# Kernel optimization log

Measured on AMD Instinct MI355X. Metric: run time of the kernel, lower is better.

## Reference

```python
import jax, jax.numpy as jnp
import numpy as np

N = 100000
E = 1600000
D_IN, H1, H2 = 64, 128, 64
ATT = 32


def _mean_aggregate(feat, src, dst, num_nodes):
    # gather source features per edge, scatter-sum to destinations, divide by in-degree
    summed = jax.ops.segment_sum(feat[src], dst, num_segments=num_nodes)  # [N, d]
    deg = jax.ops.segment_sum(jnp.ones((src.shape[0],), feat.dtype), dst, num_segments=num_nodes)
    return summed / jnp.maximum(deg, 1.0)[:, None]


def setup_inputs() -> dict:
    key = jax.random.key(0)
    ks = jax.random.split(key, 16)
    x = jax.random.normal(ks[0], (N, D_IN), dtype=jnp.float32)
    edge_index = jax.random.randint(ks[1], (2, E), 0, N, dtype=jnp.int64)

    def lin(k, fan_in, fan_out):
        bound = 1.0 / np.sqrt(fan_in)
        return jax.random.uniform(k, (fan_in, fan_out), jnp.float32, -bound, bound)

    params = {
        'W1_l': lin(ks[2], D_IN, H1), 'W1_r': lin(ks[3], D_IN, H1),
        'b1': jnp.zeros((H1,), jnp.float32),
        'W2_l': lin(ks[4], H1, H2), 'W2_r': lin(ks[5], H1, H2),
        'b2': jnp.zeros((H2,), jnp.float32),
        'Wa': lin(ks[6], H2, ATT), 'ba': jnp.zeros((ATT,), jnp.float32),
        'ctx': jax.random.normal(ks[7], (ATT,), jnp.float32),
        'Wc1': lin(ks[8], H2, H2 // 2), 'bc1': jnp.zeros((H2 // 2,), jnp.float32),
        'Wc2': lin(ks[9], H2 // 2, 1), 'bc2': jnp.zeros((1,), jnp.float32),
    }
    return {'x': x, 'edge_index': edge_index, **params}


def reference(x, edge_index, W1_l, W1_r, b1, W2_l, W2_r, b2, Wa, ba, ctx, Wc1, bc1, Wc2, bc2):
    src, dst = edge_index[0], edge_index[1]
    ionm_alerts = x[:, -1]  # [N]

    # GraphSAGE layer 1 (mean aggr): lin_l(mean_neighbors) + lin_r(x_self)
    agg1 = _mean_aggregate(x, src, dst, N)
    h = jax.nn.relu(agg1 @ W1_l + b1 + x @ W1_r)  # [N, H1]
    # F.dropout(training=False) -> identity

    # GraphSAGE layer 2
    agg2 = _mean_aggregate(h, src, dst, N)
    h = jax.nn.relu(agg2 @ W2_l + b2 + h @ W2_r)  # [N, H2]

    # attention with IONM alert boost (+0.4)
    scores = jnp.tanh(h @ Wa + ba)            # [N, ATT]
    w = scores @ ctx + ionm_alerts * 0.4       # [N]
    w = jax.nn.softmax(w, axis=0)
    h = h * w[:, None]

    pooled = jnp.mean(h, axis=0, keepdims=True)  # [1, H2]

    # classifier head (Dropout identity in eval)
    z = jax.nn.relu(pooled @ Wc1 + bc1)
    return jax.nn.sigmoid(z @ Wc2 + bc2)  # [1, 1]
```

## Files before the change

### kernel.cpp

```cpp
#include <hip/hip_runtime.h>
#include <math.h>

#define N_NODES 100000
#define E_EDGES 1600000
#define D_IN 64
#define HID1 128
#define HID2 64
#define ATT 32
#define CAP 64
#define AT_STRIDE 136
#define NRANGE 4
#define RNODES (N_NODES / NRANGE)
#define NPART 64
#define XCAST_BLOCKS ((N_NODES * 16 + 255) / 256)
#define SCAT_BLOCKS 1024

typedef unsigned int uint32;
typedef unsigned short ushort;
typedef __attribute__((ext_vector_type(8))) short short8;
typedef __attribute__((ext_vector_type(4))) float float4v;

#define NTL(p) __builtin_nontemporal_load(&(p))

__device__ inline uint32 bf16rn(float f){ uint32 u = __float_as_uint(f); return (u + 0x7fffu + ((u >> 16) & 1u)) >> 16; }
__device__ inline uint32 packbf2(float a, float b){ return bf16rn(a) | (bf16rn(b) << 16); }

#if __has_builtin(__builtin_amdgcn_cvt_f32_fp8) && __has_builtin(__builtin_amdgcn_cvt_pk_fp8_f32)
#define HW_FP8 1
#endif

__device__ inline uint32 fp8_enc_sw(float f){
    float a = fabsf(f);
    uint32 s = (__float_as_uint(f) >> 24) & 0x80u;
    if (!(a >= 0.001953125f)) return s;
    if (a > 448.f) return s | 0x7Eu;
    if (a < 0.015625f){
        uint32 c = (uint32)rintf(a * 512.f);
        return s | c;
    }
    int e; float m = frexpf(a, &e);
    int E = e - 1;
    float mant = 2.f * m;
    uint32 mc = (uint32)rintf((mant - 1.f) * 8.f);
    uint32 Ec = (uint32)(E + 7);
    if (mc == 8u){ mc = 0u; Ec += 1u; }
    if (Ec >= 16u || (Ec == 15u && mc > 6u)) return s | 0x7Eu;
    return s | (Ec << 3) | mc;
}

__device__ inline float fp8_dec_sw(uint32 c){
    uint32 s = (c & 0x80u) << 24;
    uint32 E = (c >> 3) & 0xFu, m = c & 7u;
    float v;
    if (E == 0) v = (float)m * 0.001953125f;
    else v = __uint_as_float(((E + 120u) << 23) | (m << 20));
    return __uint_as_float(__float_as_uint(v) | s);
}

__device__ inline uint32 enc4(float a, float b, float c, float d){
#ifdef HW_FP8
    int r = __builtin_amdgcn_cvt_pk_fp8_f32(a, b, 0, false);
    r = __builtin_amdgcn_cvt_pk_fp8_f32(c, d, r, true);
    return (uint32)r;
#else
    return fp8_enc_sw(a) | (fp8_enc_sw(b) << 8) | (fp8_enc_sw(c) << 16) | (fp8_enc_sw(d) << 24);
#endif
}

__device__ inline void dec4acc(uint32 w, float& a0, float& a1, float& a2, float& a3){
#ifdef HW_FP8
    a0 += __builtin_amdgcn_cvt_f32_fp8((int)w, 0);
    a1 += __builtin_amdgcn_cvt_f32_fp8((int)w, 1);
    a2 += __builtin_amdgcn_cvt_f32_fp8((int)w, 2);
    a3 += __builtin_amdgcn_cvt_f32_fp8((int)w, 3);
#else
    a0 += fp8_dec_sw(w & 0xffu);
    a1 += fp8_dec_sw((w >> 8) & 0xffu);
    a2 += fp8_dec_sw((w >> 16) & 0xffu);
    a3 += fp8_dec_sw(w >> 24);
#endif
}

__global__ void k_mega(const float* __restrict__ x,
                       const int* __restrict__ src, const int* __restrict__ dst,
                       const float* __restrict__ W1l, const float* __restrict__ W1r,
                       const float* __restrict__ W2l, const float* __restrict__ W2r,
                       uint32* __restrict__ xb, uint32* __restrict__ xq,
                       uint32* __restrict__ vq,
                       ushort* __restrict__ wt1g, ushort* __restrict__ wt2g,
                       int* __restrict__ cnt, int* __restrict__ ssrc){
    int b = blockIdx.x, t = threadIdx.x;
    if (b < XCAST_BLOCKS){
        int i = b * 256 + t;
        if (i < N_NODES * 16){
            float4v v = NTL(((const float4v*)x)[i]);
            xb[2 * i]     = packbf2(v.x, v.y);
            xb[2 * i + 1] = packbf2(v.z, v.w);
            xq[i] = enc4(v.x, v.y, v.z, v.w);
        }
        return;
    }
    if (b < XCAST_BLOCKS + 2){
        int sub = b - XCAST_BLOCKS;
        ushort* dstp = (sub == 0) ? wt1g : wt2g;
        for (int idx = t; idx < 128 * 128; idx += 256){
            int nn = idx >> 7, kk = idx & 127;
            float v;
            if (sub == 0) v = (kk < 64) ? W1l[kk * 128 + nn] : W1r[(kk - 64) * 128 + nn];
            else          v = (nn < 64) ? W2l[kk * 64 + nn]  : W2r[kk * 64 + (nn - 64)];
            dstp[nn * 128 + kk] = (ushort)bf16rn(v);
        }
        if (sub == 0){
            if (t < 16) xq[(size_t)N_NODES * 16 + t] = 0u;
            else if (t < 32) vq[(size_t)N_NODES * 16 + (t - 16)] = 0u;
        }
        return;
    }
    int rel = b - (XCAST_BLOCKS + 2);
    int range = rel & (NRANGE - 1);
    int blk   = rel >> 2;
    int lo = range * RNODES, hi = lo + RNODES;
    int stride = (SCAT_BLOCKS >> 2) * 256;
    for (int i = blk * 256 + t; i < E_EDGES; i += stride){
        int d = NTL(dst[i]);
        if (d >= lo && d < hi){
            int pos = atomicAdd(&cnt[d], 1);
            if (pos < CAP) ssrc[d * CAP + pos] = NTL(src[i]);
        }
    }
}

__device__ inline void gather8_fp8(const uint32* __restrict__ tab,
                                   const int* __restrict__ ssrc,
                                   const int* __restrict__ cnt,
                                   int n0, int lane,
                                   float acc[8][4], int cct[8]){
    int q = lane >> 4, p = lane & 15;
    int nn = n0 + (lane & 7);
    int ccl_ = cnt[nn];
    int cc[8];
    #pragma unroll
    for (int j = 0; j < 8; j++){
        int c = __shfl(ccl_, j, 64);
        cct[j] = c;
        cc[j] = min(c, CAP);
    }
    #pragma unroll
    for (int j = 0; j < 8; j++){ acc[j][0] = acc[j][1] = acc[j][2] = acc[j][3] = 0.f; }
    int cmax = 0;
    #pragma unroll
    for (int j = 0; j < 8; j++) cmax = max(cmax, cc[j]);
    if (cmax == 0) return;
    int se[8];
    #pragma unroll
    for (int j = 0; j < 8; j++){
        se[j] = (lane < cc[j]) ? NTL(ssrc[(n0 + j) * CAP + lane]) : N_NODES;
    }
    int iters = (cmax + 3) >> 2;
    uint32 w[8];
    #pragma unroll
    for (int j = 0; j < 8; j++){
        int s = __shfl(se[j], q, 64);
        w[j] = tab[(uint32)s * 16u + p];
    }
    for (int it = 0; it < iters; it++){
        uint32 wn[8];
        bool more = (it + 1 < iters);
        int idxn = (it + 1) * 4 + q;
        if (more){
            #pragma unroll
            for (int j = 0; j < 8; j++){
                int s = __shfl(se[j], idxn, 64);
                wn[j] = tab[(uint32)s * 16u + p];
            }
        }
        #pragma unroll
        for (int j = 0; j < 8; j++)
            dec4acc(w[j], acc[j][0], acc[j][1], acc[j][2], acc[j][3]);
        if (more){
            #pragma unroll
            for (int j = 0; j < 8; j++) w[j] = wn[j];
        }
    }
    #pragma unroll
    for (int j = 0; j < 8; j++){
        acc[j][0] += __shfl_xor(acc[j][0], 16, 64); acc[j][1] += __shfl_xor(acc[j][1], 16, 64);
        acc[j][2] += __shfl_xor(acc[j][2], 16, 64); acc[j][3] += __shfl_xor(acc[j][3], 16, 64);
        acc[j][0] += __shfl_xor(acc[j][0], 32, 64); acc[j][1] += __shfl_xor(acc[j][1], 32, 64);
        acc[j][2] += __shfl_xor(acc[j][2], 32, 64); acc[j][3] += __shfl_xor(acc[j][3], 32, 64);
    }
}

__global__ __launch_bounds__(256) void k_layer1(
    const uint32* __restrict__ xq, const uint32* __restrict__ xb,
    const int* __restrict__ ssrc, const int* __restrict__ cnt,
    const ushort* __restrict__ wt1g, const ushort* __restrict__ wt2g,
    const float* __restrict__ b1, const float* __restrict__ b2,
    uint32* __restrict__ vq, float* __restrict__ r2f){
    __shared__ ushort smem[2 * 32 * AT_STRIDE];
    ushort* at  = smem;
    ushort* at2 = smem + 32 * AT_STRIDE;
    float* vstage = (float*)smem;
    int t = threadIdx.x, wave = t >> 6, lane = t & 63;
    int nb0 = blockIdx.x * 32;
    int n0 = nb0 + wave * 8;

    int m0 = t >> 3, ch = t & 7;
    uint4 xval = *(const uint4*)&xb[(size_t)(nb0 + m0) * 32 + ch * 4];

    float acc[8][4]; int cct[8];
    gather8_fp8(xq, ssrc, cnt, n0, lane, acc, cct);
    int p = lane & 15;
    if (lane < 16){
        #pragma unroll
        for (int j = 0; j < 8; j++){
            float inv = 1.f / fmaxf((float)cct[j], 1.f);
            uint2 o;
            o.x = packbf2(acc[j][0] * inv, acc[j][1] * inv);
            o.y = packbf2(acc[j][2] * inv, acc[j][3] * inv);
            *(uint2*)&at[(wave * 8 + j) * AT_STRIDE + 4 * p] = o;
        }
    }
    *(uint4*)((uint32*)(at + m0 * AT_STRIDE + 64) + ch * 4) = xval;
    __syncthreads();

    int cidx = lane & 15, quad = lane >> 4;
    int mt = wave >> 1;
    int nbase = (wave & 1) * 64;
    float4v c[4];
    #pragma unroll
    for (int nt = 0; nt < 4; nt++) c[nt] = (float4v){0.f,0.f,0.f,0.f};
    #pragma unroll
    for (int kt = 0; kt < 4; kt++){
        short8 a = *(short8*)(at + ((mt * 16 + cidx) * AT_STRIDE + kt * 32 + quad * 8));
        #pragma unroll
        for (int nt = 0; nt < 4; nt++){
            short8 b = *(const short8*)(wt1g + ((nbase + nt * 16 + cidx) * 128 + kt * 32 + quad * 8));
            c[nt] = __builtin_amdgcn_mfma_f32_16x16x32_bf16(a, b, c[nt], 0, 0, 0);
        }
    }
    #pragma unroll
    for (int nt = 0; nt < 4; nt++){
        float bb = b1[nbase + nt * 16 + cidx];
        #pragma unroll
        for (int i = 0; i < 4; i++){
            int row = quad * 4 + i;
            at2[(mt * 16 + row) * AT_STRIDE + nbase + nt * 16 + cidx] =
                (ushort)bf16rn(fmaxf(c[nt][i] + bb, 0.f));
        }
    }
    __syncthreads();
    #pragma unroll
    for (int nt = 0; nt < 4; nt++) c[nt] = (float4v){0.f,0.f,0.f,0.f};
    #pragma unroll
    for (int kt = 0; kt < 4; kt++){
        short8 a = *(short8*)(at2 + ((mt * 16 + cidx) * AT_STRIDE + kt * 32 + quad * 8));
        #pragma unroll
        for (int nt = 0; nt < 4; nt++){
            short8 b = *(const short8*)(wt2g + ((nbase + nt * 16 + cidx) * 128 + kt * 32 + quad * 8));
            c[nt] = __builtin_amdgcn_mfma_f32_16x16x32_bf16(a, b, c[nt], 0, 0, 0);
        }
    }
    if (nbase == 0){
        #pragma unroll
        for (int nt = 0; nt < 4; nt++){
            #pragma unroll
            for (int i = 0; i < 4; i++){
                int row = quad * 4 + i;
                vstage[(mt * 16 + row) * 65 + nt * 16 + cidx] = c[nt][i];
            }
        }
    } else {
        #pragma unroll
        for (int nt = 0; nt < 4; nt++){
            float bb = b2[nt * 16 + cidx];
            #pragma unroll
            for (int i = 0; i < 4; i++){
                int row = quad * 4 + i;
                size_t node = nb0 + mt * 16 + row;
                r2f[node * 64 + nt * 16 + cidx] = c[nt][i] + bb;
            }
        }
    }
    __syncthreads();
    {
        int m = t >> 3, u = t & 7;
        float f0 = vstage[m * 65 + 8 * u],     f1 = vstage[m * 65 + 8 * u + 1];
        float f2 = vstage[m * 65 + 8 * u + 2], f3 = vstage[m * 65 + 8 * u + 3];
        float f4 = vstage[m * 65 + 8 * u + 4], f5 = vstage[m * 65 + 8 * u + 5];
        float f6 = vstage[m * 65 + 8 * u + 6], f7 = vstage[m * 65 + 8 * u + 7];
        vq[(size_t)(nb0 + m) * 16 + 2 * u]     = enc4(f0, f1, f2, f3);
        vq[(size_t)(nb0 + m) * 16 + 2 * u + 1] = enc4(f4, f5, f6, f7);
    }
}

__global__ __launch_bounds__(256) void k_gather2f(
    const float* __restrict__ x, const uint32* __restrict__ vq,
    const int* __restrict__ ssrc, const int* __restrict__ cnt,
    const float* __restrict__ r2f,
    const float* __restrict__ Wa, const float* __restrict__ ba, const float* __restrict__ ctx,
    float* __restrict__ pooledP, float* __restrict__ Zpart){
    __shared__ float sh2[32][68];
    __shared__ float sew[32];
    __shared__ float sp[4][64];
    int t = threadIdx.x, wave = t >> 6, lane = t & 63;
    int bn0 = blockIdx.x * 32;
    int n0 = bn0 + wave * 8;
    float acc[8][4]; int cct[8];
    gather8_fp8(vq, ssrc, cnt, n0, lane, acc, cct);
    int p = lane & 15;
    if (lane < 16){
        #pragma unroll
        for (int j = 0; j < 8; j++){
            size_t nj = n0 + j;
            float inv = 1.f / fmaxf((float)cct[j], 1.f);
            float4v rr = NTL(*(const float4v*)&r2f[nj * 64 + 4 * p]);
            float4v hv;
            hv.x = fmaxf(acc[j][0] * inv + rr.x, 0.f);
            hv.y = fmaxf(acc[j][1] * inv + rr.y, 0.f);
            hv.z = fmaxf(acc[j][2] * inv + rr.z, 0.f);
            hv.w = fmaxf(acc[j][3] * inv + rr.w, 0.f);
            *(float4v*)&sh2[wave * 8 + j][4 * p] = hv;
        }
    }
    __syncthreads();
    int node = t >> 3;
    int c0 = (t & 7) * 4;
    float s0 = ba[c0], s1 = ba[c0 + 1], s2 = ba[c0 + 2], s3 = ba[c0 + 3];
    #pragma unroll 8
    for (int j = 0; j < 64; j++){
        float hv = sh2[node][j];
        s0 += hv * Wa[j * ATT + c0];
        s1 += hv * Wa[j * ATT + c0 + 1];
        s2 += hv * Wa[j * ATT + c0 + 2];
        s3 += hv * Wa[j * ATT + c0 + 3];
    }
    float pa = tanhf(s0) * ctx[c0] + tanhf(s1) * ctx[c0 + 1]
             + tanhf(s2) * ctx[c0 + 2] + tanhf(s3) * ctx[c0 + 3];
    #pragma unroll
    for (int off = 4; off >= 1; off >>= 1) pa += __shfl_down(pa, off, 8);
    if ((t & 7) == 0){
        int n = bn0 + node;
        float w = pa + NTL(x[(size_t)n * 64 + 63]) * 0.4f;
        sew[node] = expf(w);
    }
    __syncthreads();
    int j = t & 63, q = t >> 6;
    float p4 = 0.f;
    #pragma unroll
    for (int m = 0; m < 8; m++) p4 += sh2[q * 8 + m][j] * sew[q * 8 + m];
    sp[q][j] = p4;
    __syncthreads();
    if (t < 64){
        float s = sp[0][t] + sp[1][t] + sp[2][t] + sp[3][t];
        atomicAdd(&pooledP[(blockIdx.x & (NPART - 1)) * 64 + t], s);
    }
    if (t == 64){
        float z = 0.f;
        #pragma unroll
        for (int m = 0; m < 32; m++) z += sew[m];
        atomicAdd(&Zpart[blockIdx.x & (NPART - 1)], z);
    }
}

__global__ void k_final(const float* __restrict__ pooledP, const float* __restrict__ Zpart,
                        const float* __restrict__ Wc1, const float* __restrict__ bc1,
                        const float* __restrict__ Wc2, const float* __restrict__ bc2,
                        float* __restrict__ out){
    __shared__ float sp[64], sz[32];
    __shared__ float Zs;
    int t = threadIdx.x;
    float s = 0.f;
    for (int q = 0; q < NPART; q++) s += pooledP[q * 64 + t];
    if (t == 0){
        float z = 0.f;
        for (int q = 0; q < NPART; q++) z += Zpart[q];
        Zs = z;
    }
    __syncthreads();
    float scale = 1.0f / (Zs * (float)N_NODES);
    sp[t] = s * scale;
    __syncthreads();
    if (t < 32){
        float a = bc1[t];
        #pragma unroll 8
        for (int j = 0; j < 64; j++) a += sp[j] * Wc1[j * 32 + t];
        sz[t] = fmaxf(a, 0.f);
    }
    __syncthreads();
    if (t == 0){
        float a = bc2[0];
        #pragma unroll
        for (int i = 0; i < 32; i++) a += sz[i] * Wc2[i];
        out[0] = 1.0f / (1.0f + expf(-a));
    }
}

extern "C" void kernel_launch(void* const* d_in, const int* in_sizes, int n_in,
                              void* d_out, int out_size, void* d_ws, size_t ws_size,
                              hipStream_t stream) {
    const float* x   = (const float*)d_in[0];
    const int*   ei  = (const int*)d_in[1];
    const int*   src = ei;
    const int*   dst = ei + E_EDGES;
    const float* W1l = (const float*)d_in[2];
    const float* W1r = (const float*)d_in[3];
    const float* b1  = (const float*)d_in[4];
    const float* W2l = (const float*)d_in[5];
    const float* W2r = (const float*)d_in[6];
    const float* b2  = (const float*)d_in[7];
    const float* Wa  = (const float*)d_in[8];
    const float* ba  = (const float*)d_in[9];
    const float* ctx = (const float*)d_in[10];
    const float* Wc1 = (const float*)d_in[11];
    const float* bc1 = (const float*)d_in[12];
    const float* Wc2 = (const float*)d_in[13];
    const float* bc2 = (const float*)d_in[14];

    char* p = (char*)d_ws;
    int* cnt    = (int*)p;                 p += (size_t)N_NODES * 4;
    int* ssrc   = (int*)p;                 p += (size_t)N_NODES * CAP * 4;
    uint32* xb  = (uint32*)p;              p += (size_t)N_NODES * 32 * 4;
    uint32* xq  = (uint32*)p;              p += (size_t)(N_NODES + 1) * 16 * 4;
    uint32* vq  = (uint32*)p;              p += (size_t)(N_NODES + 1) * 16 * 4;
    float* r2f  = (float*)p;               p += (size_t)N_NODES * 64 * 4;
    ushort* wt1g = (ushort*)p;             p += 128 * 128 * 2;
    ushort* wt2g = (ushort*)p;             p += 128 * 128 * 2;
    float* pooledP = (float*)p;            p += NPART * 64 * 4;
    float* Zpart   = (float*)p;            p += NPART * 4;

    hipMemsetAsync(cnt, 0, (size_t)N_NODES * 4, stream);
    hipMemsetAsync(pooledP, 0, (NPART * 64 + NPART) * 4, stream);

    k_mega<<<XCAST_BLOCKS + 2 + SCAT_BLOCKS, 256, 0, stream>>>(
        x, src, dst, W1l, W1r, W2l, W2r, xb, xq, vq, wt1g, wt2g, cnt, ssrc);

    k_layer1<<<(N_NODES + 31) / 32, 256, 0, stream>>>(xq, xb, ssrc, cnt,
                                                      wt1g, wt2g, b1, b2, vq, r2f);
    k_gather2f<<<(N_NODES + 31) / 32, 256, 0, stream>>>(x, vq, ssrc, cnt, r2f,
                                                        Wa, ba, ctx, pooledP, Zpart);
    k_final<<<1, 64, 0, stream>>>(pooledP, Zpart, Wc1, bc1, Wc2, bc2, (float*)d_out);
}
```

Measured before the change: 341.9 us.

## Fuse final head into gather kernel via ticket, drop memset, prefetch indices deeper

The final classifier head moves into the last block of k_gather2f, which is picked with an atomic ticket, so the separate k_final launch goes away. The pooled and Z partial buffers are now zeroed inside k_layer1 block 0, which replaces one hipMemsetAsync. The fp8 neighbour gather now loads source indices straight from ssrc, two iterations ahead, instead of reading them all up front and broadcasting them with shuffles. This cuts launch and memset overhead and shuffle traffic, at the cost of a threadfence and atomic per block and more scattered index loads.

```diff
diff --git a/kernel.cpp b/kernel.cpp
--- a/kernel.cpp
+++ b/kernel.cpp
@@ -88,7 +88,8 @@
                        uint32* __restrict__ xb, uint32* __restrict__ xq,
                        uint32* __restrict__ vq,
                        ushort* __restrict__ wt1g, ushort* __restrict__ wt2g,
-                       int* __restrict__ cnt, int* __restrict__ ssrc){
+                       int* __restrict__ cnt, int* __restrict__ ssrc,
+                       int* __restrict__ ticket){
     int b = blockIdx.x, t = threadIdx.x;
     if (b < XCAST_BLOCKS){
         int i = b * 256 + t;
@@ -113,6 +114,7 @@
         if (sub == 0){
             if (t < 16) xq[(size_t)N_NODES * 16 + t] = 0u;
             else if (t < 32) vq[(size_t)N_NODES * 16 + (t - 16)] = 0u;
+            else if (t == 32) *ticket = 0;
         }
         return;
     }
@@ -151,35 +153,50 @@
     #pragma unroll
     for (int j = 0; j < 8; j++) cmax = max(cmax, cc[j]);
     if (cmax == 0) return;
-    int se[8];
+    int iters = (cmax + 3) >> 2;
+
+    uint32 w[8];
+    int sB[8];
     #pragma unroll
     for (int j = 0; j < 8; j++){
-        se[j] = (lane < cc[j]) ? NTL(ssrc[(n0 + j) * CAP + lane]) : N_NODES;
-    }
-    int iters = (cmax + 3) >> 2;
-    uint32 w[8];
+        int sv = ssrc[(n0 + j) * CAP + q];
+        int s = (q < cc[j]) ? sv : N_NODES;
+        w[j] = tab[(uint32)s * 16u + p];
+    }
     #pragma unroll
     for (int j = 0; j < 8; j++){
-        int s = __shfl(se[j], q, 64);
-        w[j] = tab[(uint32)s * 16u + p];
+        int ii = 4 + q;
+        int sv = ssrc[(n0 + j) * CAP + (ii < CAP ? ii : 0)];
+        sB[j] = (ii < cc[j]) ? sv : N_NODES;
     }
     for (int it = 0; it < iters; it++){
-        uint32 wn[8];
-        bool more = (it + 1 < iters);
-        int idxn = (it + 1) * 4 + q;
-        if (more){
+        int sN[8];
+        bool m2 = (it + 2) < iters;
+        if (m2){
+            int ii = (it + 2) * 4 + q;
             #pragma unroll
             for (int j = 0; j < 8; j++){
-                int s = __shfl(se[j], idxn, 64);
-                wn[j] = tab[(uint32)s * 16u + p];
+                int sv = ssrc[(n0 + j) * CAP + ii];
+                sN[j] = (ii < cc[j]) ? sv : N_NODES;
             }
+        }
+        uint32 wN[8];
+        bool m1 = (it + 1) < iters;
+        if (m1){
+            #pragma unroll
+            for (int j = 0; j < 8; j++)
+                wN[j] = tab[(uint32)sB[j] * 16u + p];
         }
         #pragma unroll
         for (int j = 0; j < 8; j++)
             dec4acc(w[j], acc[j][0], acc[j][1], acc[j][2], acc[j][3]);
-        if (more){
-            #pragma unroll
-            for (int j = 0; j < 8; j++) w[j] = wn[j];
+        if (m1){
+            #pragma unroll
+            for (int j = 0; j < 8; j++) w[j] = wN[j];
+        }
+        if (m2){
+            #pragma unroll
+            for (int j = 0; j < 8; j++) sB[j] = sN[j];
         }
     }
     #pragma unroll
@@ -196,12 +213,16 @@
     const int* __restrict__ ssrc, const int* __restrict__ cnt,
     const ushort* __restrict__ wt1g, const ushort* __restrict__ wt2g,
     const float* __restrict__ b1, const float* __restrict__ b2,
-    uint32* __restrict__ vq, float* __restrict__ r2f){
+    uint32* __restrict__ vq, float* __restrict__ r2f,
+    float* __restrict__ pzero){
     __shared__ ushort smem[2 * 32 * AT_STRIDE];
     ushort* at  = smem;
     ushort* at2 = smem + 32 * AT_STRIDE;
     float* vstage = (float*)smem;
     int t = threadIdx.x, wave = t >> 6, lane = t & 63;
+    if (blockIdx.x == 0){
+        for (int i = t; i < NPART * 65; i += 256) pzero[i] = 0.f;
+    }
     int nb0 = blockIdx.x * 32;
     int n0 = nb0 + wave * 8;
 
@@ -299,7 +320,10 @@
     const int* __restrict__ ssrc, const int* __restrict__ cnt,
     const float* __restrict__ r2f,
     const float* __restrict__ Wa, const float* __restrict__ ba, const float* __restrict__ ctx,
-    float* __restrict__ pooledP, float* __restrict__ Zpart){
+    float* __restrict__ pooledP, float* __restrict__ Zpart,
+    const float* __restrict__ Wc1, const float* __restrict__ bc1,
+    const float* __restrict__ Wc2, const float* __restrict__ bc2,
+    float* __restrict__ out, int* __restrict__ ticket){
     __shared__ float sh2[32][68];
     __shared__ float sew[32];
     __shared__ float sp[4][64];
@@ -361,38 +385,44 @@
         for (int m = 0; m < 32; m++) z += sew[m];
         atomicAdd(&Zpart[blockIdx.x & (NPART - 1)], z);
     }
-}
-
-__global__ void k_final(const float* __restrict__ pooledP, const float* __restrict__ Zpart,
-                        const float* __restrict__ Wc1, const float* __restrict__ bc1,
-                        const float* __restrict__ Wc2, const float* __restrict__ bc2,
-                        float* __restrict__ out){
-    __shared__ float sp[64], sz[32];
-    __shared__ float Zs;
-    int t = threadIdx.x;
-    float s = 0.f;
-    for (int q = 0; q < NPART; q++) s += pooledP[q * 64 + t];
+    __threadfence();
+    __shared__ int lastBlk;
     if (t == 0){
-        float z = 0.f;
-        for (int q = 0; q < NPART; q++) z += Zpart[q];
-        Zs = z;
-    }
-    __syncthreads();
-    float scale = 1.0f / (Zs * (float)N_NODES);
-    sp[t] = s * scale;
-    __syncthreads();
-    if (t < 32){
-        float a = bc1[t];
-        #pragma unroll 8
-        for (int j = 0; j < 64; j++) a += sp[j] * Wc1[j * 32 + t];
-        sz[t] = fmaxf(a, 0.f);
-    }
-    __syncthreads();
-    if (t == 0){
-        float a = bc2[0];
-        #pragma unroll
-        for (int i = 0; i < 32; i++) a += sz[i] * Wc2[i];
-        out[0] = 1.0f / (1.0f + expf(-a));
+        int v = atomicAdd(ticket, 1);
+        lastBlk = (v == (int)gridDim.x - 1) ? 1 : 0;
+    }
+    __syncthreads();
+    if (lastBlk){
+        __shared__ float fsp[64], fsz[32];
+        __shared__ float Zs;
+        if (t < 64){
+            float s = 0.f;
+            for (int qq = 0; qq < NPART; qq++)
+                s += __hip_atomic_load(&pooledP[qq * 64 + t], __ATOMIC_RELAXED, __HIP_MEMORY_SCOPE_AGENT);
+            fsp[t] = s;
+            if (t == 0){
+                float z = 0.f;
+                for (int qq = 0; qq < NPART; qq++)
+                    z += __hip_atomic_load(&Zpart[qq], __ATOMIC_RELAXED, __HIP_MEMORY_SCOPE_AGENT);
+                Zs = z;
+            }
+        }
+        __syncthreads();
+        if (t < 64) fsp[t] *= 1.0f / (Zs * (float)N_NODES);
+        __syncthreads();
+        if (t < 32){
+            float a = bc1[t];
+            #pragma unroll 8
+            for (int jj = 0; jj < 64; jj++) a += fsp[jj] * Wc1[jj * 32 + t];
+            fsz[t] = fmaxf(a, 0.f);
+        }
+        __syncthreads();
+        if (t == 0){
+            float a = bc2[0];
+            #pragma unroll
+            for (int i = 0; i < 32; i++) a += fsz[i] * Wc2[i];
+            out[0] = 1.0f / (1.0f + expf(-a));
+        }
     }
 }
 
@@ -428,16 +458,17 @@
     ushort* wt2g = (ushort*)p;             p += 128 * 128 * 2;
     float* pooledP = (float*)p;            p += NPART * 64 * 4;
     float* Zpart   = (float*)p;            p += NPART * 4;
+    int* ticket    = (int*)p;              p += 16;
 
     hipMemsetAsync(cnt, 0, (size_t)N_NODES * 4, stream);
-    hipMemsetAsync(pooledP, 0, (NPART * 64 + NPART) * 4, stream);
 
     k_mega<<<XCAST_BLOCKS + 2 + SCAT_BLOCKS, 256, 0, stream>>>(
-        x, src, dst, W1l, W1r, W2l, W2r, xb, xq, vq, wt1g, wt2g, cnt, ssrc);
+        x, src, dst, W1l, W1r, W2l, W2r, xb, xq, vq, wt1g, wt2g, cnt, ssrc, ticket);
 
     k_layer1<<<(N_NODES + 31) / 32, 256, 0, stream>>>(xq, xb, ssrc, cnt,
-                                                      wt1g, wt2g, b1, b2, vq, r2f);
+                                                      wt1g, wt2g, b1, b2, vq, r2f, pooledP);
     k_gather2f<<<(N_NODES + 31) / 32, 256, 0, stream>>>(x, vq, ssrc, cnt, r2f,
-                                                        Wa, ba, ctx, pooledP, Zpart);
-    k_final<<<1, 64, 0, stream>>>(pooledP, Zpart, Wc1, bc1, Wc2, bc2, (float*)d_out);
-}
+                                                        Wa, ba, ctx, pooledP, Zpart,
+                                                        Wc1, bc1, Wc2, bc2,
+                                                        (float*)d_out, ticket);
+}
```

Measured after the change: 676.8 us. +97.9%, slower.
